# Kernel tuning notes

Hardware: AMD Instinct MI355X
Metric: run time of the kernel (lower is better)

Reference implementation:

```python
import jax, jax.numpy as jnp
import numpy as np

EPS = 1e-06


def elu_plus_one(x):
    # F.elu(x) + 1 == exp(x) for x < 0, x + 1 for x >= 0 (alpha=1)
    return jnp.where(x > 0, x + 1.0, jnp.exp(jnp.minimum(x, 0.0)))


def safe_divide(a, b, eps=EPS):
    return a / (b + eps)


def setup_inputs() -> dict:
    key0 = jax.random.key(0)
    kq, kk, kv, kM, kz = jax.random.split(key0, 5)
    B, H, S, D = 4, 16, 4096, 128
    query = jax.random.normal(kq, (B, H, S, D), dtype=jnp.float32)
    key = jax.random.normal(kk, (B, H, S, D), dtype=jnp.float32)
    value = jax.random.normal(kv, (B, H, S, D), dtype=jnp.float32)
    M = jax.random.normal(kM, (B, H, D, D), dtype=jnp.float32)
    z = jax.random.uniform(kz, (B, H, D, 1), dtype=jnp.float32)
    return {"query": query, "key": key, "value": value, "M": M, "z": z}


def reference(query, key, value, M, z):
    # --- update (delta rule) ---
    sigma_k = elu_plus_one(key)                       # [B,H,S,D]
    mem_pred = jnp.einsum('bhsd,bhde->bhse', sigma_k, M)   # sigma(K) @ M
    normalizer = jnp.einsum('bhsd,bhdo->bhso', sigma_k, z) # sigma(K) @ z -> [B,H,S,1]
    delta_v = value - safe_divide(mem_pred, normalizer)
    M_new = M + jnp.einsum('bhsd,bhse->bhde', sigma_k, delta_v)  # sigma(K)^T @ delta_V
    z_new = z + jnp.sum(sigma_k, axis=2)[..., None]              # [B,H,D,1]

    # --- retrieve with updated memory ---
    sigma_q = elu_plus_one(query)
    mem_out = jnp.einsum('bhsd,bhde->bhse', sigma_q, M_new)
    norm_q = jnp.einsum('bhsd,bhdo->bhso', sigma_q, z_new)
    out = safe_divide(mem_out, norm_q)                # [B,H,S,D]
    return out, M_new, z_new
```

## Files before the change

### kernel.cpp

```cpp
#include <hip/hip_runtime.h>
#include <math.h>

#define D 128
#define EPS 1e-6f
#define SKR_LD 136
#define SKT_LD 40
#define DV_LD  40
#define SKR_SZ (32 * SKR_LD)
#define SKT_SZ (128 * SKT_LD)

typedef __attribute__((ext_vector_type(8))) short short8;
typedef __attribute__((ext_vector_type(4))) float f32x4;
typedef unsigned short ushort_t;
typedef unsigned long long u64;

__device__ __forceinline__ float elu1(float x) {
    float e = __expf(fminf(x, 0.f));
    return x > 0.f ? x + 1.f : e;
}
__device__ __forceinline__ unsigned short bf16rne(float f) {
    unsigned u = __builtin_bit_cast(unsigned, f);
    u += 0x7FFFu + ((u >> 16) & 1u);
    return (unsigned short)(u >> 16);
}
__device__ __forceinline__ u64 pack4(float a, float b, float c, float d) {
    return (u64)bf16rne(a) | ((u64)bf16rne(b) << 16) |
           ((u64)bf16rne(c) << 32) | ((u64)bf16rne(d) << 48);
}

__global__ __launch_bounds__(512, 4)
void k_update(const float* __restrict__ key, const float* __restrict__ value,
              const float* __restrict__ M, const float* __restrict__ z,
              float* __restrict__ pM, float* __restrict__ pz, int S)
{
    __shared__ alignas(16) ushort_t skR[SKR_SZ];
    __shared__ alignas(16) ushort_t skT[SKT_SZ];
    __shared__ alignas(16) ushort_t dvT[128 * DV_LD];
    __shared__ float normsh[32];

    const int t  = threadIdx.x;
    const int bh = blockIdx.x, ch = blockIdx.y, NCH = gridDim.y;
    const int SC = S / NCH, NB = SC / 32, s0g = ch * SC;

    const int w = t >> 6, g = (t >> 4) & 3, m = t & 15;
    const int c2 = t & 63;

    const float* Kb = key   + (size_t)bh * S * D;
    const float* Vb = value + (size_t)bh * S * D;
    const float* Mb = M + (size_t)bh * D * D;
    const float* zb = z + (size_t)bh * D;

    const float zr0 = zb[2 * c2], zr1 = zb[2 * c2 + 1];

    short8 Bf[4];
    #pragma unroll
    for (int ks = 0; ks < 4; ++ks) {
        short8 f;
        #pragma unroll
        for (int j = 0; j < 8; ++j)
            f[j] = (short)bf16rne(Mb[(size_t)(32 * ks + 8 * g + j) * D + 16 * w + m]);
        Bf[ks] = f;
    }

    f32x4 acc[8];
    #pragma unroll
    for (int dt = 0; dt < 8; ++dt) acc[dt] = 0.f;
    float zacc0 = 0.f, zacc1 = 0.f;

    auto STAGE = [&](const float2* kr) {
        float sv0[4], sv1[4];
        #pragma unroll
        for (int i = 0; i < 4; ++i) { sv0[i] = elu1(kr[i].x); sv1[i] = elu1(kr[i].y); }
        #pragma unroll
        for (int i = 0; i < 4; ++i)
            *(unsigned*)&skR[(4 * w + i) * SKR_LD + 2 * c2] =
                (unsigned)bf16rne(sv0[i]) | ((unsigned)bf16rne(sv1[i]) << 16);
        *(u64*)&skT[(2 * c2) * SKT_LD + 4 * w]     = pack4(sv0[0], sv0[1], sv0[2], sv0[3]);
        *(u64*)&skT[(2 * c2 + 1) * SKT_LD + 4 * w] = pack4(sv1[0], sv1[1], sv1[2], sv1[3]);
        float p[4];
        #pragma unroll
        for (int i = 0; i < 4; ++i) {
            p[i] = sv0[i] * zr0 + sv1[i] * zr1;
            zacc0 += sv0[i]; zacc1 += sv1[i];
        }
        #pragma unroll
        for (int mask = 32; mask >= 1; mask >>= 1) {
            p[0] += __shfl_xor(p[0], mask, 64);
            p[1] += __shfl_xor(p[1], mask, 64);
            p[2] += __shfl_xor(p[2], mask, 64);
            p[3] += __shfl_xor(p[3], mask, 64);
        }
        int l = t & 63;
        if (l < 4) {
            float pv = l == 0 ? p[0] : l == 1 ? p[1] : l == 2 ? p[2] : p[3];
            normsh[4 * w + l] = pv + EPS;
        }
    };

    float2 kr[4];
    #pragma unroll
    for (int i = 0; i < 4; ++i)
        kr[i] = *(const float2*)&Kb[(size_t)(s0g + 4 * w + i) * D + 2 * c2];
    STAGE(kr);
    if (NB > 1) {
        #pragma unroll
        for (int i = 0; i < 4; ++i)
            kr[i] = *(const float2*)&Kb[(size_t)(s0g + 32 + 4 * w + i) * D + 2 * c2];
    }
    float vn[2][4];
    #pragma unroll
    for (int st = 0; st < 2; ++st)
        #pragma unroll
        for (int r = 0; r < 4; ++r)
            vn[st][r] = Vb[(size_t)(s0g + 16 * st + 4 * g + r) * D + 16 * w + m];
    __syncthreads();

    for (int b = 0; b < NB; ++b) {
        const int sbat = s0g + 32 * b;

        float vv[2][4];
        #pragma unroll
        for (int st = 0; st < 2; ++st)
            #pragma unroll
            for (int r = 0; r < 4; ++r) vv[st][r] = vn[st][r];

        if (b + 1 < NB) {
            #pragma unroll
            for (int st = 0; st < 2; ++st)
                #pragma unroll
                for (int r = 0; r < 4; ++r)
                    vn[st][r] = Vb[(size_t)(sbat + 32 + 16 * st + 4 * g + r) * D + 16 * w + m];
        }

        f32x4 mp[2];
        mp[0] = 0.f; mp[1] = 0.f;
        #pragma unroll
        for (int st = 0; st < 2; ++st)
            #pragma unroll
            for (int ks = 0; ks < 4; ++ks) {
                short8 a = *(short8*)&skR[(16 * st + m) * SKR_LD + 32 * ks + 8 * g];
                mp[st] = __builtin_amdgcn_mfma_f32_16x16x32_bf16(a, Bf[ks], mp[st], 0, 0, 0);
            }

        #pragma unroll
        for (int st = 0; st < 2; ++st) {
            float dv[4];
            #pragma unroll
            for (int r = 0; r < 4; ++r)
                dv[r] = vv[st][r] - mp[st][r] / normsh[16 * st + 4 * g + r];
            *(u64*)&dvT[(16 * w + m) * DV_LD + 16 * st + 4 * g] =
                pack4(dv[0], dv[1], dv[2], dv[3]);
        }
        asm volatile("" ::: "memory");

        short8 bfr = *(short8*)&dvT[(16 * w + m) * DV_LD + 8 * g];

        #pragma unroll
        for (int dt = 0; dt < 8; ++dt) {
            short8 a2 = *(short8*)&skT[(16 * dt + m) * SKT_LD + 8 * g];
            acc[dt] = __builtin_amdgcn_mfma_f32_16x16x32_bf16(a2, bfr, acc[dt], 0, 0, 0);
        }

        __syncthreads();

        if (b + 1 < NB) {
            STAGE(kr);
            if (b + 2 < NB) {
                #pragma unroll
                for (int i = 0; i < 4; ++i)
                    kr[i] = *(const float2*)&Kb[(size_t)(sbat + 64 + 4 * w + i) * D + 2 * c2];
            }
        }
        __syncthreads();
    }

    float* pMb = pM + ((size_t)bh * NCH + ch) * (D * D);
    #pragma unroll
    for (int dt = 0; dt < 8; ++dt)
        #pragma unroll
        for (int r = 0; r < 4; ++r)
            pMb[(size_t)(16 * dt + 4 * g + r) * D + 16 * w + m] = acc[dt][r];

    float* zsc = (float*)skR;
    zsc[w * 128 + 2 * c2]     = zacc0;
    zsc[w * 128 + 2 * c2 + 1] = zacc1;
    __syncthreads();
    if (t < 128) {
        float a = 0.f;
        #pragma unroll
        for (int r = 0; r < 8; ++r) a += zsc[r * 128 + t];
        pz[((size_t)bh * NCH + ch) * D + t] = a;
    }
}

__global__ void k_reduce(const float* __restrict__ M, const float* __restrict__ z,
                         const float* __restrict__ pM, const float* __restrict__ pz,
                         float* __restrict__ Mnew, float* __restrict__ znew, int NCH)
{
    const int bh = blockIdx.x, sl = blockIdx.y, t = threadIdx.x;
    const size_t baseM = (size_t)bh * D * D;
    for (int i = sl * 2048 + t; i < (sl + 1) * 2048; i += 256) {
        float a = M[baseM + i];
        for (int c = 0; c < NCH; ++c) a += pM[((size_t)bh * NCH + c) * (D * D) + i];
        Mnew[baseM + i] = a;
    }
    if (sl == 0 && t < D) {
        float a = z[(size_t)bh * D + t];
        for (int c = 0; c < NCH; ++c) a += pz[((size_t)bh * NCH + c) * D + t];
        znew[(size_t)bh * D + t] = a;
    }
}

__global__ __launch_bounds__(256, 2)
void k_retrieve(const float* __restrict__ query, const float* __restrict__ Mnew,
                const float* __restrict__ znew, float* __restrict__ out, int S)
{
    __shared__ alignas(16) ushort_t sqR[2][32 * SKR_LD];
    __shared__ float normsh[2][32];

    const int t  = threadIdx.x;
    const int bh = blockIdx.x, ch = blockIdx.y, NCH = gridDim.y;
    const int SC = S / NCH;
    const int NB = SC / 32;
    const int s0g = ch * SC;

    const int w = t >> 6, g = (t >> 4) & 3, m = t & 15;
    const int sb = t >> 5, db = t & 31;

    const float* Qb = query + (size_t)bh * S * D;
    const float* Mb = Mnew + (size_t)bh * D * D;
    const float* zb = znew + (size_t)bh * D;
    float*       Ob = out + (size_t)bh * S * D;

    float zr[4];
    #pragma unroll
    for (int j = 0; j < 4; ++j) zr[j] = zb[4 * db + j];

    short8 Bf[4][2];
    #pragma unroll
    for (int ks = 0; ks < 4; ++ks)
        #pragma unroll
        for (int p = 0; p < 2; ++p) {
            short8 f;
            #pragma unroll
            for (int j = 0; j < 8; ++j)
                f[j] = (short)bf16rne(Mb[(size_t)(32 * ks + 8 * g + j) * D + 16 * (2 * w + p) + m]);
            Bf[ks][p] = f;
        }

    auto STAGE_PROC = [&](const float4* qreg, int bu) {
        float sv[4][4];
        #pragma unroll
        for (int js = 0; js < 4; ++js) {
            sv[js][0] = elu1(qreg[js].x); sv[js][1] = elu1(qreg[js].y);
            sv[js][2] = elu1(qreg[js].z); sv[js][3] = elu1(qreg[js].w);
        }
        #pragma unroll
        for (int js = 0; js < 4; ++js)
            *(u64*)&sqR[bu][(4 * sb + js) * SKR_LD + 4 * db] =
                pack4(sv[js][0], sv[js][1], sv[js][2], sv[js][3]);
        float np[4];
        #pragma unroll
        for (int js = 0; js < 4; ++js)
            np[js] = sv[js][0] * zr[0] + sv[js][1] * zr[1] +
                     sv[js][2] * zr[2] + sv[js][3] * zr[3];
        #pragma unroll
        for (int mask = 16; mask >= 1; mask >>= 1) {
            np[0] += __shfl_xor(np[0], mask, 64);
            np[1] += __shfl_xor(np[1], mask, 64);
            np[2] += __shfl_xor(np[2], mask, 64);
            np[3] += __shfl_xor(np[3], mask, 64);
        }
        if (db < 4) {
            float v = db == 0 ? np[0] : db == 1 ? np[1] : db == 2 ? np[2] : np[3];
            normsh[bu][4 * sb + db] = v + EPS;
        }
    };

    {
        float4 qreg[4];
        #pragma unroll
        for (int js = 0; js < 4; ++js)
            qreg[js] = *(const float4*)&Qb[(size_t)(s0g + 4 * sb + js) * D + 4 * db];
        STAGE_PROC(qreg, 0);
    }
    __syncthreads();

    for (int b = 0; b < NB; ++b) {
        const int bu = b & 1;
        float4 qreg[4];
        if (b + 1 < NB) {
            #pragma unroll
            for (int js = 0; js < 4; ++js)
                qreg[js] = *(const float4*)&Qb[(size_t)(s0g + 32 * (b + 1) + 4 * sb + js) * D + 4 * db];
        }

        f32x4 mp[2][2];
        #pragma unroll
        for (int st = 0; st < 2; ++st)
            #pragma unroll
            for (int p = 0; p < 2; ++p) mp[st][p] = 0.f;
        #pragma unroll
        for (int st = 0; st < 2; ++st)
            #pragma unroll
            for (int ks = 0; ks < 4; ++ks) {
                short8 a = *(short8*)&sqR[bu][(16 * st + m) * SKR_LD + 32 * ks + 8 * g];
                #pragma unroll
                for (int p = 0; p < 2; ++p)
                    mp[st][p] = __builtin_amdgcn_mfma_f32_16x16x32_bf16(a, Bf[ks][p], mp[st][p], 0, 0, 0);
            }

        #pragma unroll
        for (int st = 0; st < 2; ++st)
            #pragma unroll
            for (int r = 0; r < 4; ++r) {
                float rn = 1.f / normsh[bu][16 * st + 4 * g + r];
                #pragma unroll
                for (int p = 0; p < 2; ++p)
                    Ob[(size_t)(s0g + 32 * b + 16 * st + 4 * g + r) * D + 16 * (2 * w + p) + m] =
                        mp[st][p][r] * rn;
            }

        if (b + 1 < NB) STAGE_PROC(qreg, (b + 1) & 1);
        __syncthreads();
    }
}

extern "C" void kernel_launch(void* const* d_in, const int* in_sizes, int n_in,
                              void* d_out, int out_size, void* d_ws, size_t ws_size,
                              hipStream_t stream)
{
    const float* q = (const float*)d_in[0];
    const float* k = (const float*)d_in[1];
    const float* v = (const float*)d_in[2];
    const float* M = (const float*)d_in[3];
    const float* z = (const float*)d_in[4];

    const int BH = in_sizes[3] / (D * D);
    const int S  = in_sizes[0] / (BH * D);

    float* out  = (float*)d_out;
    float* Mnew = out + (size_t)BH * S * D;
    float* znew = Mnew + (size_t)BH * D * D;

    int NCH = 16;
    const size_t per_set = (size_t)BH * (D * D + D) * sizeof(float);
    while (NCH > 1 && (size_t)NCH * per_set > ws_size) NCH >>= 1;

    float* pM;
    float* pz;
    if ((size_t)NCH * per_set <= ws_size) {
        pM = (float*)d_ws;
        pz = pM + (size_t)NCH * BH * D * D;
    } else {
        NCH = 1;
        pM = Mnew;
        pz = znew;
    }

    dim3 gridA(BH, NCH);
    k_update<<<gridA, 512, 0, stream>>>(k, v, M, z, pM, pz, S);
    dim3 gridB(BH, 8);
    k_reduce<<<gridB, 256, 0, stream>>>(M, z, pM, pz, Mnew, znew, NCH);
    dim3 gridC(BH, 8);
    k_retrieve<<<gridC, 256, 0, stream>>>(q, Mnew, znew, out, S);
}
```

Before: 180.1 us.

## Reassociate delta-rule update into K^T V and normalized K^T K products times M

Rewrites M_new = M + K^T V - (K^T diag(1/n) K) M, so the update kernel no longer needs the per-batch sigma(K)@M product that depended on M. Each batch now accumulates two Gram-style products from one shared sigma(K)^T tile, using double-buffered swizzled LDS tiles and a single barrier per iteration. A new k_gm kernel applies the correction G@M with a split-bf16 (hi+lo) G to preserve accuracy. Partial sums are staged in the output buffer instead of the workspace, and the chunk count is fixed. The trade-off is doubled MFMA and partial-sum traffic in the update kernel plus an extra kernel launch.

```diff
diff --git a/kernel.cpp b/kernel.cpp
--- a/kernel.cpp
+++ b/kernel.cpp
@@ -3,11 +3,9 @@
 
 #define D 128
 #define EPS 1e-6f
+#define TLD 40
+#define TSZ (128 * TLD)
 #define SKR_LD 136
-#define SKT_LD 40
-#define DV_LD  40
-#define SKR_SZ (32 * SKR_LD)
-#define SKT_SZ (128 * SKT_LD)
 
 typedef __attribute__((ext_vector_type(8))) short short8;
 typedef __attribute__((ext_vector_type(4))) float f32x4;
@@ -23,20 +21,27 @@
     u += 0x7FFFu + ((u >> 16) & 1u);
     return (unsigned short)(u >> 16);
 }
+__device__ __forceinline__ float bf2f(unsigned short h) {
+    unsigned u = (unsigned)h << 16;
+    return __builtin_bit_cast(float, u);
+}
 __device__ __forceinline__ u64 pack4(float a, float b, float c, float d) {
     return (u64)bf16rne(a) | ((u64)bf16rne(b) << 16) |
            ((u64)bf16rne(c) << 32) | ((u64)bf16rne(d) << 48);
 }
+__device__ __forceinline__ int swzs(int f, int u) {
+    return TLD * f + 8 * (u ^ (f & 3) ^ ((f >> 2) & 3));
+}
 
 __global__ __launch_bounds__(512, 4)
 void k_update(const float* __restrict__ key, const float* __restrict__ value,
-              const float* __restrict__ M, const float* __restrict__ z,
-              float* __restrict__ pM, float* __restrict__ pz, int S)
-{
-    __shared__ alignas(16) ushort_t skR[SKR_SZ];
-    __shared__ alignas(16) ushort_t skT[SKT_SZ];
-    __shared__ alignas(16) ushort_t dvT[128 * DV_LD];
-    __shared__ float normsh[32];
+              const float* __restrict__ z,
+              float* __restrict__ pP, float* __restrict__ pG,
+              float* __restrict__ pz, int S)
+{
+    __shared__ alignas(16) ushort_t sT[2 * TSZ];
+    __shared__ alignas(16) ushort_t vT[2 * TSZ];
+    __shared__ float nrm[2][32];
 
     const int t  = threadIdx.x;
     const int bh = blockIdx.x, ch = blockIdx.y, NCH = gridDim.y;
@@ -47,40 +52,28 @@
 
     const float* Kb = key   + (size_t)bh * S * D;
     const float* Vb = value + (size_t)bh * S * D;
-    const float* Mb = M + (size_t)bh * D * D;
     const float* zb = z + (size_t)bh * D;
 
-    const float zr0 = zb[2 * c2], zr1 = zb[2 * c2 + 1];
-
-    short8 Bf[4];
-    #pragma unroll
-    for (int ks = 0; ks < 4; ++ks) {
-        short8 f;
-        #pragma unroll
-        for (int j = 0; j < 8; ++j)
-            f[j] = (short)bf16rne(Mb[(size_t)(32 * ks + 8 * g + j) * D + 16 * w + m]);
-        Bf[ks] = f;
-    }
-
-    f32x4 acc[8];
-    #pragma unroll
-    for (int dt = 0; dt < 8; ++dt) acc[dt] = 0.f;
+    const float2 zr = *(const float2*)&zb[2 * c2];
+
+    f32x4 accP[8], accG[8];
+    #pragma unroll
+    for (int dt = 0; dt < 8; ++dt) { accP[dt] = 0.f; accG[dt] = 0.f; }
     float zacc0 = 0.f, zacc1 = 0.f;
 
-    auto STAGE = [&](const float2* kr) {
+    auto STAGE = [&](const float2* kr, const float2* vr, int buf) {
         float sv0[4], sv1[4];
         #pragma unroll
         for (int i = 0; i < 4; ++i) { sv0[i] = elu1(kr[i].x); sv1[i] = elu1(kr[i].y); }
-        #pragma unroll
-        for (int i = 0; i < 4; ++i)
-            *(unsigned*)&skR[(4 * w + i) * SKR_LD + 2 * c2] =
-                (unsigned)bf16rne(sv0[i]) | ((unsigned)bf16rne(sv1[i]) << 16);
-        *(u64*)&skT[(2 * c2) * SKT_LD + 4 * w]     = pack4(sv0[0], sv0[1], sv0[2], sv0[3]);
-        *(u64*)&skT[(2 * c2 + 1) * SKT_LD + 4 * w] = pack4(sv1[0], sv1[1], sv1[2], sv1[3]);
+        const int u = w >> 1, h4 = 4 * (w & 1);
+        *(u64*)&sT[buf * TSZ + swzs(2 * c2,     u) + h4] = pack4(sv0[0], sv0[1], sv0[2], sv0[3]);
+        *(u64*)&sT[buf * TSZ + swzs(2 * c2 + 1, u) + h4] = pack4(sv1[0], sv1[1], sv1[2], sv1[3]);
+        *(u64*)&vT[buf * TSZ + swzs(2 * c2,     u) + h4] = pack4(vr[0].x, vr[1].x, vr[2].x, vr[3].x);
+        *(u64*)&vT[buf * TSZ + swzs(2 * c2 + 1, u) + h4] = pack4(vr[0].y, vr[1].y, vr[2].y, vr[3].y);
         float p[4];
         #pragma unroll
         for (int i = 0; i < 4; ++i) {
-            p[i] = sv0[i] * zr0 + sv1[i] * zr1;
+            p[i] = sv0[i] * zr.x + sv1[i] * zr.y;
             zacc0 += sv0[i]; zacc1 += sv1[i];
         }
         #pragma unroll
@@ -93,95 +86,70 @@
         int l = t & 63;
         if (l < 4) {
             float pv = l == 0 ? p[0] : l == 1 ? p[1] : l == 2 ? p[2] : p[3];
-            normsh[4 * w + l] = pv + EPS;
+            nrm[buf][4 * w + l] = 1.f / (pv + EPS);
         }
     };
 
-    float2 kr[4];
-    #pragma unroll
-    for (int i = 0; i < 4; ++i)
+    float2 kr[4], vr[4];
+    #pragma unroll
+    for (int i = 0; i < 4; ++i) {
         kr[i] = *(const float2*)&Kb[(size_t)(s0g + 4 * w + i) * D + 2 * c2];
-    STAGE(kr);
+        vr[i] = *(const float2*)&Vb[(size_t)(s0g + 4 * w + i) * D + 2 * c2];
+    }
+    STAGE(kr, vr, 0);
     if (NB > 1) {
         #pragma unroll
-        for (int i = 0; i < 4; ++i)
+        for (int i = 0; i < 4; ++i) {
             kr[i] = *(const float2*)&Kb[(size_t)(s0g + 32 + 4 * w + i) * D + 2 * c2];
-    }
-    float vn[2][4];
-    #pragma unroll
-    for (int st = 0; st < 2; ++st)
-        #pragma unroll
-        for (int r = 0; r < 4; ++r)
-            vn[st][r] = Vb[(size_t)(s0g + 16 * st + 4 * g + r) * D + 16 * w + m];
+            vr[i] = *(const float2*)&Vb[(size_t)(s0g + 32 + 4 * w + i) * D + 2 * c2];
+        }
+    }
     __syncthreads();
 
     for (int b = 0; b < NB; ++b) {
-        const int sbat = s0g + 32 * b;
-
-        float vv[2][4];
-        #pragma unroll
-        for (int st = 0; st < 2; ++st)
-            #pragma unroll
-            for (int r = 0; r < 4; ++r) vv[st][r] = vn[st][r];
+        const int cur = b & 1;
+
+        float rn[8];
+        #pragma unroll
+        for (int j = 0; j < 8; ++j) rn[j] = nrm[cur][8 * g + j];
+        short8 bv = *(short8*)&vT[cur * TSZ + swzs(16 * w + m, g)];
+        short8 bs = *(short8*)&sT[cur * TSZ + swzs(16 * w + m, g)];
+        short8 bg;
+        #pragma unroll
+        for (int j = 0; j < 8; ++j) bg[j] = (short)bf16rne(bf2f((unsigned short)bs[j]) * rn[j]);
+        #pragma unroll
+        for (int dt = 0; dt < 8; ++dt) {
+            short8 a = *(short8*)&sT[cur * TSZ + swzs(16 * dt + m, g)];
+            accP[dt] = __builtin_amdgcn_mfma_f32_16x16x32_bf16(a, bv, accP[dt], 0, 0, 0);
+            accG[dt] = __builtin_amdgcn_mfma_f32_16x16x32_bf16(a, bg, accG[dt], 0, 0, 0);
+        }
 
         if (b + 1 < NB) {
-            #pragma unroll
-            for (int st = 0; st < 2; ++st)
+            STAGE(kr, vr, cur ^ 1);
+            if (b + 2 < NB) {
+                const int snx = s0g + 32 * (b + 2);
                 #pragma unroll
-                for (int r = 0; r < 4; ++r)
-                    vn[st][r] = Vb[(size_t)(sbat + 32 + 16 * st + 4 * g + r) * D + 16 * w + m];
-        }
-
-        f32x4 mp[2];
-        mp[0] = 0.f; mp[1] = 0.f;
-        #pragma unroll
-        for (int st = 0; st < 2; ++st)
-            #pragma unroll
-            for (int ks = 0; ks < 4; ++ks) {
-                short8 a = *(short8*)&skR[(16 * st + m) * SKR_LD + 32 * ks + 8 * g];
-                mp[st] = __builtin_amdgcn_mfma_f32_16x16x32_bf16(a, Bf[ks], mp[st], 0, 0, 0);
+                for (int i = 0; i < 4; ++i) {
+                    kr[i] = *(const float2*)&Kb[(size_t)(snx + 4 * w + i) * D + 2 * c2];
+                    vr[i] = *(const float2*)&Vb[(size_t)(snx + 4 * w + i) * D + 2 * c2];
+                }
             }
-
-        #pragma unroll
-        for (int st = 0; st < 2; ++st) {
-            float dv[4];
-            #pragma unroll
-            for (int r = 0; r < 4; ++r)
-                dv[r] = vv[st][r] - mp[st][r] / normsh[16 * st + 4 * g + r];
-            *(u64*)&dvT[(16 * w + m) * DV_LD + 16 * st + 4 * g] =
-                pack4(dv[0], dv[1], dv[2], dv[3]);
-        }
-        asm volatile("" ::: "memory");
-
-        short8 bfr = *(short8*)&dvT[(16 * w + m) * DV_LD + 8 * g];
-
-        #pragma unroll
-        for (int dt = 0; dt < 8; ++dt) {
-            short8 a2 = *(short8*)&skT[(16 * dt + m) * SKT_LD + 8 * g];
-            acc[dt] = __builtin_amdgcn_mfma_f32_16x16x32_bf16(a2, bfr, acc[dt], 0, 0, 0);
-        }
-
-        __syncthreads();
-
-        if (b + 1 < NB) {
-            STAGE(kr);
-            if (b + 2 < NB) {
-                #pragma unroll
-                for (int i = 0; i < 4; ++i)
-                    kr[i] = *(const float2*)&Kb[(size_t)(sbat + 64 + 4 * w + i) * D + 2 * c2];
-            }
-        }
-        __syncthreads();
-    }
-
-    float* pMb = pM + ((size_t)bh * NCH + ch) * (D * D);
+        }
+        asm volatile("s_waitcnt lgkmcnt(0)\n\ts_barrier" ::: "memory");
+    }
+
+    float* pPb = pP + ((size_t)bh * NCH + ch) * (D * D);
+    float* pGb = pG + ((size_t)bh * NCH + ch) * (D * D);
     #pragma unroll
     for (int dt = 0; dt < 8; ++dt)
         #pragma unroll
-        for (int r = 0; r < 4; ++r)
-            pMb[(size_t)(16 * dt + 4 * g + r) * D + 16 * w + m] = acc[dt][r];
-
-    float* zsc = (float*)skR;
+        for (int r = 0; r < 4; ++r) {
+            pPb[(size_t)(16 * dt + 4 * g + r) * D + 16 * w + m] = accP[dt][r];
+            pGb[(size_t)(16 * dt + 4 * g + r) * D + 16 * w + m] = accG[dt][r];
+        }
+
+    __syncthreads();
+    float* zsc = (float*)sT;
     zsc[w * 128 + 2 * c2]     = zacc0;
     zsc[w * 128 + 2 * c2 + 1] = zacc1;
     __syncthreads();
@@ -193,22 +161,83 @@
     }
 }
 
-__global__ void k_reduce(const float* __restrict__ M, const float* __restrict__ z,
-                         const float* __restrict__ pM, const float* __restrict__ pz,
-                         float* __restrict__ Mnew, float* __restrict__ znew, int NCH)
+__global__ void k_sum(const float* __restrict__ M, const float* __restrict__ z,
+                      const float* __restrict__ pP, const float* __restrict__ pG,
+                      const float* __restrict__ pz,
+                      float* __restrict__ Mtmp, ushort_t* __restrict__ gh,
+                      ushort_t* __restrict__ gl, float* __restrict__ znew, int NCH)
 {
     const int bh = blockIdx.x, sl = blockIdx.y, t = threadIdx.x;
-    const size_t baseM = (size_t)bh * D * D;
+    const size_t base = (size_t)bh * D * D;
     for (int i = sl * 2048 + t; i < (sl + 1) * 2048; i += 256) {
-        float a = M[baseM + i];
-        for (int c = 0; c < NCH; ++c) a += pM[((size_t)bh * NCH + c) * (D * D) + i];
-        Mnew[baseM + i] = a;
+        float sp = M[base + i];
+        float sg = 0.f;
+        for (int c = 0; c < NCH; ++c) {
+            sp += pP[((size_t)bh * NCH + c) * (D * D) + i];
+            sg += pG[((size_t)bh * NCH + c) * (D * D) + i];
+        }
+        Mtmp[base + i] = sp;
+        float nG = -sg;
+        unsigned short hi = bf16rne(nG);
+        gh[base + i] = hi;
+        gl[base + i] = bf16rne(nG - bf2f(hi));
     }
     if (sl == 0 && t < D) {
         float a = z[(size_t)bh * D + t];
         for (int c = 0; c < NCH; ++c) a += pz[((size_t)bh * NCH + c) * D + t];
         znew[(size_t)bh * D + t] = a;
     }
+}
+
+__global__ __launch_bounds__(256)
+void k_gm(const float* __restrict__ M, const float* __restrict__ Mtmp,
+          const ushort_t* __restrict__ gh, const ushort_t* __restrict__ gl,
+          float* __restrict__ Mnew)
+{
+    const int bh = blockIdx.x, t = threadIdx.x;
+    const int w2 = t >> 6, g = (t >> 4) & 3, m = t & 15;
+    const float* Mb = M + (size_t)bh * D * D;
+    const float* Tb = Mtmp + (size_t)bh * D * D;
+    const ushort_t* ghb = gh + (size_t)bh * D * D;
+    const ushort_t* glb = gl + (size_t)bh * D * D;
+    float* Ob = Mnew + (size_t)bh * D * D;
+
+    f32x4 acc[8][2];
+    #pragma unroll
+    for (int dt = 0; dt < 8; ++dt)
+        #pragma unroll
+        for (int p = 0; p < 2; ++p)
+            #pragma unroll
+            for (int r = 0; r < 4; ++r)
+                acc[dt][p][r] = Tb[(size_t)(16 * dt + 4 * g + r) * D + 32 * w2 + 16 * p + m];
+
+    #pragma unroll
+    for (int ks = 0; ks < 4; ++ks) {
+        short8 bm[2];
+        #pragma unroll
+        for (int p = 0; p < 2; ++p)
+            #pragma unroll
+            for (int j = 0; j < 8; ++j)
+                bm[p][j] = (short)bf16rne(Mb[(size_t)(32 * ks + 8 * g + j) * D + 32 * w2 + 16 * p + m]);
+        #pragma unroll
+        for (int dt = 0; dt < 8; ++dt) {
+            short8 ah = *(const short8*)&ghb[(size_t)(16 * dt + m) * D + 32 * ks + 8 * g];
+            short8 al = *(const short8*)&glb[(size_t)(16 * dt + m) * D + 32 * ks + 8 * g];
+            #pragma unroll
+            for (int p = 0; p < 2; ++p) {
+                acc[dt][p] = __builtin_amdgcn_mfma_f32_16x16x32_bf16(ah, bm[p], acc[dt][p], 0, 0, 0);
+                acc[dt][p] = __builtin_amdgcn_mfma_f32_16x16x32_bf16(al, bm[p], acc[dt][p], 0, 0, 0);
+            }
+        }
+    }
+
+    #pragma unroll
+    for (int dt = 0; dt < 8; ++dt)
+        #pragma unroll
+        for (int p = 0; p < 2; ++p)
+            #pragma unroll
+            for (int r = 0; r < 4; ++r)
+                Ob[(size_t)(16 * dt + 4 * g + r) * D + 32 * w2 + 16 * p + m] = acc[dt][p][r];
 }
 
 __global__ __launch_bounds__(256, 2)
@@ -338,30 +367,24 @@
 
     const int BH = in_sizes[3] / (D * D);
     const int S  = in_sizes[0] / (BH * D);
+    const int NCH = 8;
 
     float* out  = (float*)d_out;
     float* Mnew = out + (size_t)BH * S * D;
     float* znew = Mnew + (size_t)BH * D * D;
 
-    int NCH = 16;
-    const size_t per_set = (size_t)BH * (D * D + D) * sizeof(float);
-    while (NCH > 1 && (size_t)NCH * per_set > ws_size) NCH >>= 1;
-
-    float* pM;
-    float* pz;
-    if ((size_t)NCH * per_set <= ws_size) {
-        pM = (float*)d_ws;
-        pz = pM + (size_t)NCH * BH * D * D;
-    } else {
-        NCH = 1;
-        pM = Mnew;
-        pz = znew;
-    }
+    float* pP   = out;
+    float* pG   = pP + (size_t)NCH * BH * D * D;
+    float* pz   = pG + (size_t)NCH * BH * D * D;
+    float* Mtmp = pz + (size_t)NCH * BH * D;
+    ushort_t* gh = (ushort_t*)(Mtmp + (size_t)BH * D * D);
+    ushort_t* gl = gh + (size_t)BH * D * D;
 
     dim3 gridA(BH, NCH);
-    k_update<<<gridA, 512, 0, stream>>>(k, v, M, z, pM, pz, S);
+    k_update<<<gridA, 512, 0, stream>>>(k, v, z, pP, pG, pz, S);
     dim3 gridB(BH, 8);
-    k_reduce<<<gridB, 256, 0, stream>>>(M, z, pM, pz, Mnew, znew, NCH);
+    k_sum<<<gridB, 256, 0, stream>>>(M, z, pP, pG, pz, Mtmp, gh, gl, znew, NCH);
+    k_gm<<<BH, 256, 0, stream>>>(M, Mtmp, gh, gl, Mnew);
     dim3 gridC(BH, 8);
     k_retrieve<<<gridC, 256, 0, stream>>>(q, Mnew, znew, out, S);
 }
```

New measurement: 177.7 us. Within noise of the previous version (-1.3%).
